# Kernel optimization log

Measured on AMD Instinct MI355X. Metric: run time of the kernel, lower is better.

Reference implementation:

```python
import jax, jax.numpy as jnp
import numpy as np

H = W = 256
N_VERTS = 6890
N_FACES = 13776
CHUNK = 164            # 13776 = 84 * 164
N_CHUNKS = N_FACES // CHUNK
BIG = 1e9
EPS = 1e-8


def _project(cam, verts):
    # weak-perspective: s * (xy + t); flip y into image (raster) space
    xy = cam[:, None, 0:1] * (verts[:, :, :2] + cam[:, None, 1:3])
    return jnp.concatenate([xy[..., 0:1], -xy[..., 1:2], verts[:, :, 2:3]], axis=-1)  # [B,N,3]


def _rasterize(proj, faces):
    """Z-buffered rasterization. proj [B,N,3], faces [F,3] ->
    fim [B,P] int32 (face index, -1 = background), wim [B,P,3] barycentric weights."""
    B = proj.shape[0]
    P = H * W
    tri = proj[:, faces]                                   # [B,F,3,3]
    tri_c = tri.reshape(B, N_CHUNKS, CHUNK, 3, 3).transpose(1, 0, 2, 3, 4)  # [nc,B,C,3,3]
    bases = (jnp.arange(N_CHUNKS) * CHUNK).astype(jnp.int32)
    c = (jnp.arange(H, dtype=jnp.float32) + 0.5) / H * 2.0 - 1.0   # pixel centers in [-1,1]
    py, px = jnp.meshgrid(c, c, indexing='ij')
    px = px.reshape(-1)[None, :, None]                     # [1,P,1]
    py = py.reshape(-1)[None, :, None]

    def step(carry, xs):
        zbuf, fid, wim = carry
        t, base = xs                                       # t [B,CHUNK,3,3]
        v = t[:, None]                                     # [B,1,CHUNK,3,3]
        x0, y0, z0 = v[..., 0, 0], v[..., 0, 1], v[..., 0, 2]
        x1, y1, z1 = v[..., 1, 0], v[..., 1, 1], v[..., 1, 2]
        x2, y2, z2 = v[..., 2, 0], v[..., 2, 1], v[..., 2, 2]
        denom = (y1 - y2) * (x0 - x2) + (x2 - x1) * (y0 - y2)
        inv = 1.0 / jnp.where(jnp.abs(denom) < EPS, 1.0, denom)
        w0 = ((y1 - y2) * (px - x2) + (x2 - x1) * (py - y2)) * inv   # [B,P,CHUNK]
        w1 = ((y2 - y0) * (px - x2) + (x0 - x2) * (py - y2)) * inv
        w2 = 1.0 - w0 - w1
        inside = (w0 >= 0) & (w1 >= 0) & (w2 >= 0) & (jnp.abs(denom) >= EPS)
        depth = jnp.where(inside, w0 * z0 + w1 * z1 + w2 * z2, BIG)
        loc = jnp.argmin(depth, axis=-1)                   # [B,P]
        li = loc[..., None]
        dmin = jnp.take_along_axis(depth, li, -1)[..., 0]
        b0 = jnp.take_along_axis(w0, li, -1)[..., 0]
        b1 = jnp.take_along_axis(w1, li, -1)[..., 0]
        b2 = jnp.take_along_axis(w2, li, -1)[..., 0]
        bsel = jnp.stack([b0, b1, b2], axis=-1)            # [B,P,3]
        upd = dmin < zbuf
        zbuf = jnp.where(upd, dmin, zbuf)
        fid = jnp.where(upd, base + loc.astype(jnp.int32), fid)
        wim = jnp.where(upd[..., None], bsel, wim)
        return (zbuf, fid, wim), None

    init = (jnp.full((B, P), BIG, jnp.float32),
            jnp.full((B, P), -1, jnp.int32),
            jnp.zeros((B, P, 3), jnp.float32))
    (zbuf, fid, wim), _ = jax.lax.scan(step, init, (tri_c, bases))
    return fid, wim


def _grid_sample_border(img, grid):
    # torch.nn.functional.grid_sample(bilinear, padding_mode='border', align_corners=False)
    B, C, Hh, Ww = img.shape
    ix = jnp.clip(((grid[..., 0] + 1.0) * Ww - 1.0) * 0.5, 0.0, Ww - 1.0)
    iy = jnp.clip(((grid[..., 1] + 1.0) * Hh - 1.0) * 0.5, 0.0, Hh - 1.0)
    x0 = jnp.floor(ix); y0 = jnp.floor(iy)
    wx = ix - x0; wy = iy - y0
    x0i = x0.astype(jnp.int32); y0i = y0.astype(jnp.int32)
    x1i = jnp.clip(x0i + 1, 0, Ww - 1); y1i = jnp.clip(y0i + 1, 0, Hh - 1)
    b = jnp.arange(B)[:, None, None]
    Ia = img[b, :, y0i, x0i]   # [B,H,W,C]
    Ib = img[b, :, y0i, x1i]
    Ic = img[b, :, y1i, x0i]
    Id = img[b, :, y1i, x1i]
    out = (Ia * ((1 - wx) * (1 - wy))[..., None] + Ib * (wx * (1 - wy))[..., None]
           + Ic * ((1 - wx) * wy)[..., None] + Id * (wx * wy)[..., None])
    return out.transpose(0, 3, 1, 2)


def setup_inputs() -> dict:
    key = jax.random.key(0)
    k1, k2, k3, k4, k5, k6 = jax.random.split(key, 6)
    B = 2
    return {
        'src_img': jax.random.normal(k1, (B, 3, H, W), jnp.float32),
        'src_cam': jax.random.uniform(k2, (B, 3), jnp.float32),
        'src_vertices': jax.random.normal(k3, (B, N_VERTS, 3), jnp.float32),
        'tgt_cam': jax.random.uniform(k4, (B, 3), jnp.float32),
        'tgt_vertices': jax.random.normal(k5, (B, N_VERTS, 3), jnp.float32),
        'faces': jax.random.randint(k6, (N_FACES, 3), 0, N_VERTS, jnp.int32),
    }


def reference(src_img, src_cam, src_vertices, tgt_cam, tgt_vertices, faces):
    B = src_img.shape[0]
    # source faces -> projected 2D verts; flip y back (matches src_f2verts[...,1] *= -1)
    src_proj = _project(src_cam, src_vertices)
    src_f2v = src_proj[:, faces][..., 0:2]                 # [B,F,3,2]
    src_f2v = src_f2v.at[..., 1].multiply(-1.0)
    # rasterize target mesh -> face-index map + barycentric weight map
    tgt_proj = _project(tgt_cam, tgt_vertices)
    fim, wim = _rasterize(tgt_proj, faces)                 # [B,P], [B,P,3]
    fid_clip = jnp.clip(fim, 0, N_FACES - 1)
    gathered = src_f2v[jnp.arange(B)[:, None], fid_clip]   # [B,P,3,2]
    flow = jnp.sum(wim[..., None] * gathered, axis=2)      # [B,P,2]
    flow = jnp.where((fim >= 0)[..., None], flow, -2.0)    # background off-grid
    flow = flow.reshape(B, H, W, 2)
    return _grid_sample_border(src_img, flow)
```

## Files before the change

### kernel.cpp

```cpp
#include <hip/hip_runtime.h>

#pragma clang fp contract(off)

#define HH 256
#define WW 256
#define NVERTS 6890
#define NFACES 13776
#define RASTN (NFACES + 1)
#define PAD1 14336
#define LISTSTRIDE 13824
#define RCHUNK 32
#define MAXCH 432
#define SLABS 4
#define WSUB 896
#define NITER 14
#define SLABSZ (4 * WSUB)
#define NBLK 2048
#define NWAVES (NBLK * 4)
#define BIGF 1000000000.0f
#define EPSF 1e-8f

__device__ __forceinline__ float pixc(int i) {
    return __fsub_rn(__fmul_rn(__fdiv_rn(__fadd_rn((float)i, 0.5f), 256.0f), 2.0f), 1.0f);
}

__device__ __forceinline__ unsigned int fsort(float f) {
    unsigned int u = __float_as_uint(f);
    return (u & 0x80000000u) ? ~u : (u | 0x80000000u);
}


__global__ __launch_bounds__(256) void precompute_kernel(
    const float* __restrict__ src_cam, const float* __restrict__ src_verts,
    const float* __restrict__ tgt_cam, const float* __restrict__ tgt_verts,
    const int* __restrict__ faces,
    float4* __restrict__ rast64, uchar4* __restrict__ pass1,
    float4* __restrict__ eplane,
    float4* __restrict__ flowg,
    unsigned long long* __restrict__ zbuf,
    int* __restrict__ counts, int* __restrict__ done, int* __restrict__ qcount,
    int B)
{
    int idx = blockIdx.x * blockDim.x + threadIdx.x;
    if (idx < B * HH * WW) zbuf[idx] = ~0ull;
    if (counts && idx < B * 256) { counts[idx] = 0; done[idx] = 0; }
    if (qcount && idx == 0) qcount[0] = 0;
    if (idx >= B * PAD1) return;
    int b = idx / PAD1;
    int f = idx - b * PAD1;
    if (f >= NFACES) {
        if (pass1) pass1[(size_t)b * PAD1 + f] = make_uchar4(255, 255, 0, 0);
        if (f == NFACES) {
            float4* rr = rast64 + ((size_t)b * RASTN + f) * 4;
            rr[0] = make_float4(0.0f, 0.0f, 0.0f, 0.0f);
            rr[1] = make_float4(0.0f, 0.0f, 1.0f, __int_as_float(-1));
            rr[2] = make_float4(BIGF, BIGF, BIGF, 0.0f);
            rr[3] = make_float4(0.0f, 0.0f, 0.0f, 0.0f);
        }
        return;
    }
    float4* rr = rast64 + ((size_t)b * RASTN + f) * 4;
    int i0 = faces[3*f+0], i1 = faces[3*f+1], i2 = faces[3*f+2];

    float tc0 = tgt_cam[3*b+0], tc1 = tgt_cam[3*b+1], tc2 = tgt_cam[3*b+2];
    const float* tv = tgt_verts + (size_t)b * NVERTS * 3;
    float x0 = __fmul_rn(tc0, __fadd_rn(tv[3*i0+0], tc1));
    float y0 = -__fmul_rn(tc0, __fadd_rn(tv[3*i0+1], tc2));
    float z0 = tv[3*i0+2];
    float x1 = __fmul_rn(tc0, __fadd_rn(tv[3*i1+0], tc1));
    float y1 = -__fmul_rn(tc0, __fadd_rn(tv[3*i1+1], tc2));
    float z1 = tv[3*i1+2];
    float x2 = __fmul_rn(tc0, __fadd_rn(tv[3*i2+0], tc1));
    float y2 = -__fmul_rn(tc0, __fadd_rn(tv[3*i2+1], tc2));
    float z2 = tv[3*i2+2];

    float A  = __fsub_rn(y1, y2);
    float D  = __fsub_rn(x0, x2);
    float Bc = __fsub_rn(x2, x1);
    float E_ = __fsub_rn(y0, y2);
    float denom = __fadd_rn(__fmul_rn(A, D), __fmul_rn(Bc, E_));
    bool valid = (fabsf(denom) >= EPSF);
    float inv = __fdiv_rn(1.0f, valid ? denom : 1.0f);
    float Cc = __fsub_rn(y2, y0);

    if (valid) {
        rr[0] = make_float4(x2, y2, A, Bc);
        rr[1] = make_float4(Cc, D, inv, __int_as_float(f));
        rr[2] = make_float4(z0, z1, z2, 0.0f);
    } else {
        rr[0] = make_float4(0.0f, 0.0f, 0.0f, 0.0f);
        rr[1] = make_float4(0.0f, 0.0f, 1.0f, __int_as_float(f));
        rr[2] = make_float4(BIGF, BIGF, BIGF, 0.0f);
    }
    rr[3] = make_float4(0.0f, 0.0f, 0.0f, 0.0f);

    uchar4 range;
    float4 e1, e2, e3;
    if (valid) {
        float xmn = fminf(fminf(x0, x1), x2), xmx = fmaxf(fmaxf(x0, x1), x2);
        float ymn = fminf(fminf(y0, y1), y2), ymx = fmaxf(fmaxf(y0, y1), y2);
        float S = fmaxf(fmaxf(fabsf(xmn), fabsf(xmx)),
                        fmaxf(fabsf(ymn), fabsf(ymx))) + 1.01f;
        float slop = 2e-6f * S;
        float l0 = sqrtf(D*D + E_*E_);
        float dx1v = x1 - x2, dy1v = y1 - y2;
        float l1 = sqrtf(dx1v*dx1v + dy1v*dy1v);
        float dx2v = x1 - x0, dy2v = y1 - y0;
        float l2 = sqrtf(dx2v*dx2v + dy2v*dy2v);
        float mp = fmaxf(fmaxf(l0*l1, l1*l2), l0*l2);
        float Ex = slop * mp / fabsf(denom);
        float m = Ex + slop + 1e-4f;
        float bxmn = xmn - m, bymn = ymn - m, bxmx = xmx + m, bymx = ymx + m;

        int txlo = (int)floorf((__fmul_rn(__fadd_rn(bxmn, 1.0f), 128.0f) - 15.5f) * 0.0625f);
        txlo = max(0, min(16, txlo));
        while (txlo > 0  && pixc(16*(txlo-1)+15) >= bxmn) txlo--;
        while (txlo < 16 && pixc(16*txlo+15)     <  bxmn) txlo++;
        int txhi = (int)floorf((__fmul_rn(__fadd_rn(bxmx, 1.0f), 128.0f) - 0.5f) * 0.0625f);
        txhi = max(-1, min(15, txhi));
        while (txhi < 15 && pixc(16*(txhi+1)) <= bxmx) txhi++;
        while (txhi >= 0 && pixc(16*txhi)     >  bxmx) txhi--;
        int tylo = (int)floorf((__fmul_rn(__fadd_rn(bymn, 1.0f), 128.0f) - 15.5f) * 0.0625f);
        tylo = max(0, min(16, tylo));
        while (tylo > 0  && pixc(16*(tylo-1)+15) >= bymn) tylo--;
        while (tylo < 16 && pixc(16*tylo+15)     <  bymn) tylo++;
        int tyhi = (int)floorf((__fmul_rn(__fadd_rn(bymx, 1.0f), 128.0f) - 0.5f) * 0.0625f);
        tyhi = max(-1, min(15, tyhi));
        while (tyhi < 15 && pixc(16*(tyhi+1)) <= bymx) tyhi++;
        while (tyhi >= 0 && pixc(16*tyhi)     >  bymx) tyhi--;
        if (txlo > txhi || tylo > tyhi || txlo > 15 || tylo > 15 ||
            txhi < 0 || tyhi < 0) {
            range = make_uchar4(255, 255, 0, 0);
        } else {
            range = make_uchar4((unsigned char)txlo, (unsigned char)tylo,
                                (unsigned char)txhi, (unsigned char)tyhi);
        }

        float s = (denom >= 0.0f) ? 1.0f : -1.0f;
        float gx0 = s * A,  gy0 = s * Bc;
        float gx1 = s * Cc, gy1 = s * D;
        float gx2 = s * (y0 - y1), gy2 = s * (x1 - x0);
        float b0 = -(gx0 * x2 + gy0 * y2);
        float b1 = -(gx1 * x2 + gy1 * y2);
        float b2 = fabsf(denom) - b0 - b1;
        float mm15 = 1.5f * m;
        float k0 = b0 + mm15 * l1 + 1e-6f;
        float k1 = b1 + mm15 * l0 + 1e-6f;
        float k2 = b2 + mm15 * l2 + 1e-6f;
        e1 = make_float4(gx0, gy0, k0, gx1);
        e2 = make_float4(gy1, k1, gx2, gy2);
        e3 = make_float4(k2, 0.0f, 0.0f, 0.0f);
    } else {
        range = make_uchar4(255, 255, 0, 0);
        e1 = make_float4(0.0f, 0.0f, -1.0f, 0.0f);
        e2 = make_float4(0.0f, -1.0f, 0.0f, 0.0f);
        e3 = make_float4(-1.0f, 0.0f, 0.0f, 0.0f);
    }
    if (pass1) pass1[(size_t)b * PAD1 + f] = range;
    if (eplane) {
        float4* ep = eplane + ((size_t)b * NFACES + f) * 4;
        ep[0] = e1; ep[1] = e2; ep[2] = e3;
        ep[3] = make_float4(0.0f, 0.0f, 0.0f, 0.0f);
    }

    float sc0 = src_cam[3*b+0], sc1 = src_cam[3*b+1], sc2 = src_cam[3*b+2];
    const float* sv = src_verts + (size_t)b * NVERTS * 3;
    float g0x = __fmul_rn(sc0, __fadd_rn(sv[3*i0+0], sc1));
    float g0y = __fmul_rn(sc0, __fadd_rn(sv[3*i0+1], sc2));
    float g1x = __fmul_rn(sc0, __fadd_rn(sv[3*i1+0], sc1));
    float g1y = __fmul_rn(sc0, __fadd_rn(sv[3*i1+1], sc2));
    float g2x = __fmul_rn(sc0, __fadd_rn(sv[3*i2+0], sc1));
    float g2y = __fmul_rn(sc0, __fadd_rn(sv[3*i2+1], sc2));
    size_t fo = ((size_t)b * NFACES + f) * 2;
    flowg[fo+0] = make_float4(g0x, g0y, g1x, g1y);
    flowg[fo+1] = make_float4(g2x, g2y, 0.0f, 0.0f);
}

__global__ __launch_bounds__(256) void bin_kernel(
    const uchar4* __restrict__ pass1, const float4* __restrict__ eplane,
    int* __restrict__ lists,
    int* __restrict__ counts, int* __restrict__ done,
    unsigned int* __restrict__ queue, int* __restrict__ qcount, int B)
{
    __shared__ int seg[4][WSUB];
    int tile = blockIdx.x;
    int slab = blockIdx.y;
    int b = blockIdx.z;
    int tileG = b * 256 + tile;
    int tX = tile & 15, tY = tile >> 4;
    float txmin = pixc(tX * 16), txmax = pixc(tX * 16 + 15);
    float tymin = pixc(tY * 16), tymax = pixc(tY * 16 + 15);

    int wv = threadIdx.x >> 6, lane = threadIdx.x & 63;
    const uchar4* p1 = pass1 + (size_t)b * PAD1;
    const float4* ep = eplane + (size_t)b * NFACES * 4;
    int* mylist = lists + (size_t)tileG * LISTSTRIDE;
    int wlo = slab * SLABSZ + wv * WSUB;
    int cnt = 0;

    int f0 = wlo + lane;
    uchar4 c = p1[f0];

    #pragma unroll
    for (int it = 0; it < NITER; ++it) {
        uchar4 n;
        if (it + 1 < NITER) n = p1[f0 + (it + 1) * 64];
        int f = f0 + it * 64;
        bool pass = (tX >= (int)c.x) & (tX <= (int)c.z) &
                    (tY >= (int)c.y) & (tY <= (int)c.w);
        unsigned long long m = __ballot(pass);
        if (pass) {
            int pre = __popcll(m & ((1ull << lane) - 1ull));
            seg[wv][cnt + pre] = f;
        }
        cnt += __popcll(m);
        c = n;
    }

    int outc = 0;
    for (int base = 0; base < cnt; base += 64) {
        int i = base + lane;
        int f = (i < cnt) ? seg[wv][i] : 0;
        const float4* er = ep + (size_t)f * 4;
        float4 e1 = er[0], e2 = er[1], e3 = er[2];
        float v0 = e1.x * (e1.x >= 0.0f ? txmax : txmin)
                 + e1.y * (e1.y >= 0.0f ? tymax : tymin) + e1.z;
        float v1 = e1.w * (e1.w >= 0.0f ? txmax : txmin)
                 + e2.x * (e2.x >= 0.0f ? tymax : tymin) + e2.y;
        float v2 = e2.z * (e2.z >= 0.0f ? txmax : txmin)
                 + e2.w * (e2.w >= 0.0f ? tymax : tymin) + e3.x;
        bool pass = (i < cnt) & (v0 >= 0.0f) & (v1 >= 0.0f) & (v2 >= 0.0f);
        unsigned long long m = __ballot(pass);
        if (pass) {
            int pre = __popcll(m & ((1ull << lane) - 1ull));
            seg[wv][outc + pre] = f;
        }
        outc += __popcll(m);
    }
    cnt = outc;

    int gbase = 0;
    if (lane == 0 && cnt) gbase = atomicAdd(&counts[tileG], cnt);
    gbase = __shfl(gbase, 0);
    for (int i = lane; i < cnt; i += 64) mylist[gbase + i] = seg[wv][i];

    __syncthreads();
    if (threadIdx.x < 64) {
        int isLast = 0, cc = 0;
        if (threadIdx.x == 0) {
            isLast = (atomicAdd(&done[tileG], 1) == SLABS - 1);
            if (isLast) cc = atomicAdd(&counts[tileG], 0);
        }
        isLast = __shfl(isLast, 0);
        if (isLast) {
            cc = __shfl(cc, 0);
            int padded = (cc + RCHUNK - 1) & ~(RCHUNK - 1);
            for (int i = cc + threadIdx.x; i < padded; i += 64)
                mylist[i] = NFACES;
            int nch = padded / RCHUNK;
            if (nch) {
                int qb = 0;
                if (threadIdx.x == 0) qb = atomicAdd(qcount, nch);
                qb = __shfl(qb, 0);
                for (int kk = threadIdx.x; kk < nch; kk += 64)
                    queue[qb + kk] = ((unsigned int)tileG << 10) | (unsigned int)kk;
            }
        }
    }
}

__global__ __launch_bounds__(256) void raster_kernel(
    const float* __restrict__ rast64, const int* __restrict__ lists,
    const unsigned int* __restrict__ queue, const int* __restrict__ qcount,
    unsigned long long* __restrict__ zbuf, int B)
{
    int wv = threadIdx.x >> 6, lane = threadIdx.x & 63;
    int waveId = blockIdx.x * 4 + wv;
    int qn = queue ? qcount[0] : B * 256 * MAXCH;
    qn = __builtin_amdgcn_readfirstlane(qn);

    for (int e = waveId; e < qn; e += NWAVES) {
        int tileG, k;
        if (queue) {
            unsigned int ent = queue[e];
            tileG = (int)(ent >> 10); k = (int)(ent & 1023u);
        } else {
            tileG = e / MAXCH; k = e - tileG * MAXCH;
        }
        tileG = __builtin_amdgcn_readfirstlane(tileG);
        k = __builtin_amdgcn_readfirstlane(k);
        int b = tileG >> 8, tile = tileG & 255;
        const int* lp = lists ? (lists + (size_t)tileG * LISTSTRIDE + k * RCHUNK)
                              : nullptr;
        const float* rb = rast64 + (size_t)b * RASTN * 16;

        int tX = tile & 15, tY = tile >> 4;
        int col = lane & 15, row0 = lane >> 4;
        int pxi = tX * 16 + col;
        float px = pixc(pxi);
        float py0 = pixc(tY * 16 + row0);
        float py1 = pixc(tY * 16 + row0 + 4);
        float py2 = pixc(tY * 16 + row0 + 8);
        float py3 = pixc(tY * 16 + row0 + 12);

        float z0c = BIGF, z1c = BIGF, z2c = BIGF, z3c = BIGF;
        int f0c = -1, f1c = -1, f2c = -1, f3c = -1;

        for (int j = 0; j < RCHUNK; j += 4) {
            int4 fis;
            if (lp) {
                fis = *(const int4*)(lp + j);
            } else {
                int base = k * RCHUNK + j;
                fis.x = min(base + 0, NFACES); fis.y = min(base + 1, NFACES);
                fis.z = min(base + 2, NFACES); fis.w = min(base + 3, NFACES);
            }
            #pragma unroll
            for (int q = 0; q < 4; ++q) {
                int fi = (q == 0) ? fis.x : (q == 1) ? fis.y : (q == 2) ? fis.z : fis.w;
                fi = __builtin_amdgcn_readfirstlane(fi);
                const float* r = rb + (size_t)fi * 16;
                float X2 = r[0], Y2 = r[1], A = r[2], Bc = r[3];
                float Cc = r[4], Dd = r[5], inv = r[6];
                int   fid = __float_as_int(r[7]);
                float Z0 = r[8], Z1 = r[9], Z2 = r[10];

                float dx  = __fsub_rn(px, X2);
                float Adx = __fmul_rn(A, dx);
                float Cdx = __fmul_rn(Cc, dx);
                auto evalp = [&](float py, float& zc, int& fc) {
                    float dy = __fsub_rn(py, Y2);
                    float w0 = __fmul_rn(__fadd_rn(Adx, __fmul_rn(Bc, dy)), inv);
                    float w1 = __fmul_rn(__fadd_rn(Cdx, __fmul_rn(Dd, dy)), inv);
                    float w2 = __fsub_rn(__fsub_rn(1.0f, w0), w1);
                    float d  = __fadd_rn(__fadd_rn(__fmul_rn(w0, Z0), __fmul_rn(w1, Z1)),
                                         __fmul_rn(w2, Z2));
                    float mm = fminf(fminf(w0, w1), w2);
                    bool ins = (mm >= 0.0f) & (d < zc);
                    if (ins) { zc = d; fc = fid; }
                };
                evalp(py0, z0c, f0c);
                evalp(py1, z1c, f1c);
                evalp(py2, z2c, f2c);
                evalp(py3, z3c, f3c);
            }
        }

        auto commit = [&](int rowk, float zc, int fc) {
            if (fc >= 0) {
                unsigned long long pk =
                    ((unsigned long long)fsort(zc) << 32) | (unsigned int)fc;
                int pyi = tY * 16 + row0 + rowk * 4;
                atomicMin(&zbuf[((size_t)b << 16) | (pyi << 8) | pxi], pk);
            }
        };
        commit(0, z0c, f0c);
        commit(1, z1c, f1c);
        commit(2, z2c, f2c);
        commit(3, z3c, f3c);
    }
}

__global__ __launch_bounds__(256) void resolve_kernel(
    const float* __restrict__ rast64, const float4* __restrict__ flowg,
    const unsigned long long* __restrict__ zbuf,
    const float* __restrict__ src_img, float* __restrict__ out, int B)
{
    int idx = blockIdx.x * 256 + threadIdx.x;
    if (idx >= B * HH * WW) return;
    int b = idx >> 16;
    int pix = idx & 65535;
    int pxi = pix & 255, pyi = pix >> 8;
    float px = pixc(pxi), py = pixc(pyi);

    unsigned int fid = (unsigned int)zbuf[idx];
    float fx, fy;
    if (fid != 0xFFFFFFFFu) {
        const float* r = rast64 + ((size_t)b * RASTN + fid) * 16;
        float dx = __fsub_rn(px, r[0]);
        float dy = __fsub_rn(py, r[1]);
        float w0 = __fmul_rn(__fadd_rn(__fmul_rn(r[2], dx), __fmul_rn(r[3], dy)), r[6]);
        float w1 = __fmul_rn(__fadd_rn(__fmul_rn(r[4], dx), __fmul_rn(r[5], dy)), r[6]);
        float w2 = __fsub_rn(__fsub_rn(1.0f, w0), w1);
        const float4* fg = flowg + ((size_t)b * NFACES + fid) * 2;
        float4 g0 = fg[0];
        float4 g1 = fg[1];
        fx = __fadd_rn(__fadd_rn(__fmul_rn(w0, g0.x), __fmul_rn(w1, g0.z)),
                       __fmul_rn(w2, g1.x));
        fy = __fadd_rn(__fadd_rn(__fmul_rn(w0, g0.y), __fmul_rn(w1, g0.w)),
                       __fmul_rn(w2, g1.y));
    } else {
        fx = -2.0f; fy = -2.0f;
    }

    float ix = __fmul_rn(__fsub_rn(__fmul_rn(__fadd_rn(fx, 1.0f), 256.0f), 1.0f), 0.5f);
    float iy = __fmul_rn(__fsub_rn(__fmul_rn(__fadd_rn(fy, 1.0f), 256.0f), 1.0f), 0.5f);
    ix = fminf(fmaxf(ix, 0.0f), 255.0f);
    iy = fminf(fmaxf(iy, 0.0f), 255.0f);
    float x0f = floorf(ix), y0f = floorf(iy);
    float wx = __fsub_rn(ix, x0f), wy = __fsub_rn(iy, y0f);
    int x0i = (int)x0f, y0i = (int)y0f;
    int x1i = min(x0i + 1, 255), y1i = min(y0i + 1, 255);
    float omwx = __fsub_rn(1.0f, wx), omwy = __fsub_rn(1.0f, wy);
    float wa = __fmul_rn(omwx, omwy);
    float wb = __fmul_rn(wx, omwy);
    float wc = __fmul_rn(omwx, wy);
    float wd = __fmul_rn(wx, wy);
    const float* img = src_img + (size_t)b * 3 * HH * WW;
    int o00 = y0i * WW + x0i, o01 = y0i * WW + x1i;
    int o10 = y1i * WW + x0i, o11 = y1i * WW + x1i;
    float* ob = out + (size_t)b * 3 * HH * WW + (size_t)pyi * WW + pxi;
    for (int c = 0; c < 3; ++c) {
        const float* ic = img + (size_t)c * HH * WW;
        float Ia = ic[o00], Ib = ic[o01], Ic = ic[o10], Id = ic[o11];
        float val = __fadd_rn(__fadd_rn(__fadd_rn(__fmul_rn(Ia, wa), __fmul_rn(Ib, wb)),
                                        __fmul_rn(Ic, wc)),
                              __fmul_rn(Id, wd));
        ob[(size_t)c * HH * WW] = val;
    }
}

extern "C" void kernel_launch(void* const* d_in, const int* in_sizes, int n_in,
                              void* d_out, int out_size, void* d_ws, size_t ws_size,
                              hipStream_t stream)
{
    const float* src_img   = (const float*)d_in[0];
    const float* src_cam   = (const float*)d_in[1];
    const float* src_verts = (const float*)d_in[2];
    const float* tgt_cam   = (const float*)d_in[3];
    const float* tgt_verts = (const float*)d_in[4];
    const int*   faces     = (const int*)d_in[5];
    int B = in_sizes[1] / 3;

    size_t off = 0;
    auto alloc = [&](size_t bytes) {
        size_t o = off;
        off = (off + bytes + 255) & ~(size_t)255;
        return o;
    };
    size_t rastOff = alloc((size_t)B * RASTN * 64);
    size_t p1Off   = alloc((size_t)B * PAD1 * 4);
    size_t edgOff  = alloc((size_t)B * NFACES * 64);
    size_t flowOff = alloc((size_t)B * NFACES * 2 * sizeof(float4));
    size_t zbufOff = alloc((size_t)B * HH * WW * sizeof(unsigned long long));
    size_t cntOff  = alloc((size_t)B * 256 * sizeof(int));
    size_t donOff  = alloc((size_t)B * 256 * sizeof(int));
    size_t qcOff   = alloc(sizeof(int));
    size_t quOff   = alloc((size_t)B * 256 * MAXCH * sizeof(unsigned int));
    size_t listOff = alloc((size_t)B * 256 * LISTSTRIDE * sizeof(int));
    bool binned = (off <= ws_size);

    char* ws = (char*)d_ws;
    float4* rast64 = (float4*)(ws + rastOff);
    uchar4* pass1  = binned ? (uchar4*)(ws + p1Off)  : nullptr;
    float4* eplane = binned ? (float4*)(ws + edgOff) : nullptr;
    float4* flowg  = (float4*)(ws + flowOff);
    unsigned long long* zbuf = (unsigned long long*)(ws + zbufOff);
    int* counts = binned ? (int*)(ws + cntOff) : nullptr;
    int* done   = binned ? (int*)(ws + donOff) : nullptr;
    int* qcount = binned ? (int*)(ws + qcOff)  : nullptr;
    unsigned int* queue = binned ? (unsigned int*)(ws + quOff) : nullptr;
    int* lists  = binned ? (int*)(ws + listOff) : nullptr;

    int nInit = B * HH * WW;
    int nPre  = B * PAD1;
    int nMax  = nInit > nPre ? nInit : nPre;
    precompute_kernel<<<(nMax + 255) / 256, 256, 0, stream>>>(
        src_cam, src_verts, tgt_cam, tgt_verts, faces,
        rast64, pass1, eplane, flowg, zbuf, counts, done, qcount, B);
    if (binned) {
        bin_kernel<<<dim3(256, SLABS, B), 256, 0, stream>>>(
            pass1, eplane, lists, counts, done, queue, qcount, B);
    }
    raster_kernel<<<NBLK, 256, 0, stream>>>(
        (const float*)rast64, lists, queue, qcount, zbuf, B);
    resolve_kernel<<<(B * HH * WW + 255) / 256, 256, 0, stream>>>(
        (const float*)rast64, flowg, zbuf, src_img, (float*)d_out, B);
}
```

Baseline: 147.1 us.

## Add per-face min-depth culling against zbuf and reorder raster work chunk-major

Each face stores a conservative minimum depth, and the raster waves read the current zbuf values for their pixels up front. They skip a face's barycentric evaluation when no lane's depth bound could be beaten, updating that bound after each chunk. The atomic work queue is replaced by a chunk-major enumeration using a max chunk count plus the per-tile padded count, so all tiles' first chunks run first and populate zbuf early. This adds atomic loads and empty iterations for tiles with fewer chunks, and culling depends on a safe epsilon margin.

```diff
diff --git a/kernel.cpp b/kernel.cpp
--- a/kernel.cpp
+++ b/kernel.cpp
@@ -27,6 +27,12 @@
 __device__ __forceinline__ unsigned int fsort(float f) {
     unsigned int u = __float_as_uint(f);
     return (u & 0x80000000u) ? ~u : (u | 0x80000000u);
+}
+
+__device__ __forceinline__ float funsort(unsigned int u) {
+    if (u == 0xFFFFFFFFu) return BIGF;
+    unsigned int v = (u & 0x80000000u) ? (u & 0x7FFFFFFFu) : ~u;
+    return __uint_as_float(v);
 }
 
 
@@ -55,7 +61,7 @@
             rr[0] = make_float4(0.0f, 0.0f, 0.0f, 0.0f);
             rr[1] = make_float4(0.0f, 0.0f, 1.0f, __int_as_float(-1));
             rr[2] = make_float4(BIGF, BIGF, BIGF, 0.0f);
-            rr[3] = make_float4(0.0f, 0.0f, 0.0f, 0.0f);
+            rr[3] = make_float4(BIGF, 0.0f, 0.0f, 0.0f);
         }
         return;
     }
@@ -83,16 +89,20 @@
     float inv = __fdiv_rn(1.0f, valid ? denom : 1.0f);
     float Cc = __fsub_rn(y2, y0);
 
+    float fzmin = fminf(fminf(z0, z1), z2)
+                - 4e-6f * (fabsf(z0) + fabsf(z1) + fabsf(z2)) - 1e-30f;
+
     if (valid) {
         rr[0] = make_float4(x2, y2, A, Bc);
         rr[1] = make_float4(Cc, D, inv, __int_as_float(f));
         rr[2] = make_float4(z0, z1, z2, 0.0f);
+        rr[3] = make_float4(fzmin, 0.0f, 0.0f, 0.0f);
     } else {
         rr[0] = make_float4(0.0f, 0.0f, 0.0f, 0.0f);
         rr[1] = make_float4(0.0f, 0.0f, 1.0f, __int_as_float(f));
         rr[2] = make_float4(BIGF, BIGF, BIGF, 0.0f);
-    }
-    rr[3] = make_float4(0.0f, 0.0f, 0.0f, 0.0f);
+        rr[3] = make_float4(BIGF, 0.0f, 0.0f, 0.0f);
+    }
 
     uchar4 range;
     float4 e1, e2, e3;
@@ -180,7 +190,7 @@
     const uchar4* __restrict__ pass1, const float4* __restrict__ eplane,
     int* __restrict__ lists,
     int* __restrict__ counts, int* __restrict__ done,
-    unsigned int* __restrict__ queue, int* __restrict__ qcount, int B)
+    int* __restrict__ qcount, int B)
 {
     __shared__ int seg[4][WSUB];
     int tile = blockIdx.x;
@@ -257,13 +267,10 @@
             int padded = (cc + RCHUNK - 1) & ~(RCHUNK - 1);
             for (int i = cc + threadIdx.x; i < padded; i += 64)
                 mylist[i] = NFACES;
-            int nch = padded / RCHUNK;
-            if (nch) {
-                int qb = 0;
-                if (threadIdx.x == 0) qb = atomicAdd(qcount, nch);
-                qb = __shfl(qb, 0);
-                for (int kk = threadIdx.x; kk < nch; kk += 64)
-                    queue[qb + kk] = ((unsigned int)tileG << 10) | (unsigned int)kk;
+            if (threadIdx.x == 0) {
+                int nch = padded / RCHUNK;
+                if (nch) atomicMax(qcount, nch);
+                done[tileG] = padded;
             }
         }
     }
@@ -271,37 +278,54 @@
 
 __global__ __launch_bounds__(256) void raster_kernel(
     const float* __restrict__ rast64, const int* __restrict__ lists,
-    const unsigned int* __restrict__ queue, const int* __restrict__ qcount,
+    const int* __restrict__ donep, const int* __restrict__ qcount,
     unsigned long long* __restrict__ zbuf, int B)
 {
     int wv = threadIdx.x >> 6, lane = threadIdx.x & 63;
     int waveId = blockIdx.x * 4 + wv;
-    int qn = queue ? qcount[0] : B * 256 * MAXCH;
-    qn = __builtin_amdgcn_readfirstlane(qn);
+    int NT = B * 256;
+    int maxK = lists ? qcount[0] : MAXCH;
+    maxK = __builtin_amdgcn_readfirstlane(maxK);
+    int qn = maxK * NT;
 
     for (int e = waveId; e < qn; e += NWAVES) {
-        int tileG, k;
-        if (queue) {
-            unsigned int ent = queue[e];
-            tileG = (int)(ent >> 10); k = (int)(ent & 1023u);
-        } else {
-            tileG = e / MAXCH; k = e - tileG * MAXCH;
-        }
+        int k = e / NT;
+        int tileG = e - k * NT;
+        k = __builtin_amdgcn_readfirstlane(k);
         tileG = __builtin_amdgcn_readfirstlane(tileG);
-        k = __builtin_amdgcn_readfirstlane(k);
+        const int* lp = nullptr;
+        if (lists) {
+            int padded = donep[tileG];
+            if (k * RCHUNK >= padded) continue;
+            lp = lists + (size_t)tileG * LISTSTRIDE + k * RCHUNK;
+        }
         int b = tileG >> 8, tile = tileG & 255;
-        const int* lp = lists ? (lists + (size_t)tileG * LISTSTRIDE + k * RCHUNK)
-                              : nullptr;
         const float* rb = rast64 + (size_t)b * RASTN * 16;
 
         int tX = tile & 15, tY = tile >> 4;
         int col = lane & 15, row0 = lane >> 4;
         int pxi = tX * 16 + col;
         float px = pixc(pxi);
-        float py0 = pixc(tY * 16 + row0);
-        float py1 = pixc(tY * 16 + row0 + 4);
-        float py2 = pixc(tY * 16 + row0 + 8);
-        float py3 = pixc(tY * 16 + row0 + 12);
+        int ry0 = tY * 16 + row0;
+        float py0 = pixc(ry0);
+        float py1 = pixc(ry0 + 4);
+        float py2 = pixc(ry0 + 8);
+        float py3 = pixc(ry0 + 12);
+
+        size_t zbase = ((size_t)b << 16) | (size_t)pxi;
+        unsigned long long pk0 = __hip_atomic_load(
+            &zbuf[zbase | ((size_t)ry0 << 8)], __ATOMIC_RELAXED, __HIP_MEMORY_SCOPE_AGENT);
+        unsigned long long pk1 = __hip_atomic_load(
+            &zbuf[zbase | ((size_t)(ry0 + 4) << 8)], __ATOMIC_RELAXED, __HIP_MEMORY_SCOPE_AGENT);
+        unsigned long long pk2 = __hip_atomic_load(
+            &zbuf[zbase | ((size_t)(ry0 + 8) << 8)], __ATOMIC_RELAXED, __HIP_MEMORY_SCOPE_AGENT);
+        unsigned long long pk3 = __hip_atomic_load(
+            &zbuf[zbase | ((size_t)(ry0 + 12) << 8)], __ATOMIC_RELAXED, __HIP_MEMORY_SCOPE_AGENT);
+        float zb0 = funsort((unsigned int)(pk0 >> 32));
+        float zb1 = funsort((unsigned int)(pk1 >> 32));
+        float zb2 = funsort((unsigned int)(pk2 >> 32));
+        float zb3 = funsort((unsigned int)(pk3 >> 32));
+        float laneBound = fmaxf(fmaxf(zb0, zb1), fmaxf(zb2, zb3));
 
         float z0c = BIGF, z1c = BIGF, z2c = BIGF, z3c = BIGF;
         int f0c = -1, f1c = -1, f2c = -1, f3c = -1;
@@ -320,37 +344,42 @@
                 int fi = (q == 0) ? fis.x : (q == 1) ? fis.y : (q == 2) ? fis.z : fis.w;
                 fi = __builtin_amdgcn_readfirstlane(fi);
                 const float* r = rb + (size_t)fi * 16;
-                float X2 = r[0], Y2 = r[1], A = r[2], Bc = r[3];
-                float Cc = r[4], Dd = r[5], inv = r[6];
-                int   fid = __float_as_int(r[7]);
-                float Z0 = r[8], Z1 = r[9], Z2 = r[10];
-
-                float dx  = __fsub_rn(px, X2);
-                float Adx = __fmul_rn(A, dx);
-                float Cdx = __fmul_rn(Cc, dx);
-                auto evalp = [&](float py, float& zc, int& fc) {
-                    float dy = __fsub_rn(py, Y2);
-                    float w0 = __fmul_rn(__fadd_rn(Adx, __fmul_rn(Bc, dy)), inv);
-                    float w1 = __fmul_rn(__fadd_rn(Cdx, __fmul_rn(Dd, dy)), inv);
-                    float w2 = __fsub_rn(__fsub_rn(1.0f, w0), w1);
-                    float d  = __fadd_rn(__fadd_rn(__fmul_rn(w0, Z0), __fmul_rn(w1, Z1)),
-                                         __fmul_rn(w2, Z2));
-                    float mm = fminf(fminf(w0, w1), w2);
-                    bool ins = (mm >= 0.0f) & (d < zc);
-                    if (ins) { zc = d; fc = fid; }
-                };
-                evalp(py0, z0c, f0c);
-                evalp(py1, z1c, f1c);
-                evalp(py2, z2c, f2c);
-                evalp(py3, z3c, f3c);
+                float fzmin = r[12];
+                if (__any(fzmin <= laneBound)) {
+                    float X2 = r[0], Y2 = r[1], A = r[2], Bc = r[3];
+                    float Cc = r[4], Dd = r[5], inv = r[6];
+                    int   fid = __float_as_int(r[7]);
+                    float Z0 = r[8], Z1 = r[9], Z2 = r[10];
+
+                    float dx  = __fsub_rn(px, X2);
+                    float Adx = __fmul_rn(A, dx);
+                    float Cdx = __fmul_rn(Cc, dx);
+                    auto evalp = [&](float py, float& zc, int& fc) {
+                        float dy = __fsub_rn(py, Y2);
+                        float w0 = __fmul_rn(__fadd_rn(Adx, __fmul_rn(Bc, dy)), inv);
+                        float w1 = __fmul_rn(__fadd_rn(Cdx, __fmul_rn(Dd, dy)), inv);
+                        float w2 = __fsub_rn(__fsub_rn(1.0f, w0), w1);
+                        float d  = __fadd_rn(__fadd_rn(__fmul_rn(w0, Z0), __fmul_rn(w1, Z1)),
+                                             __fmul_rn(w2, Z2));
+                        float mm = fminf(fminf(w0, w1), w2);
+                        bool ins = (mm >= 0.0f) & (d < zc);
+                        if (ins) { zc = d; fc = fid; }
+                    };
+                    evalp(py0, z0c, f0c);
+                    evalp(py1, z1c, f1c);
+                    evalp(py2, z2c, f2c);
+                    evalp(py3, z3c, f3c);
+                }
             }
+            laneBound = fmaxf(fmaxf(fminf(zb0, z0c), fminf(zb1, z1c)),
+                              fmaxf(fminf(zb2, z2c), fminf(zb3, z3c)));
         }
 
         auto commit = [&](int rowk, float zc, int fc) {
             if (fc >= 0) {
                 unsigned long long pk =
                     ((unsigned long long)fsort(zc) << 32) | (unsigned int)fc;
-                int pyi = tY * 16 + row0 + rowk * 4;
+                int pyi = ry0 + rowk * 4;
                 atomicMin(&zbuf[((size_t)b << 16) | (pyi << 8) | pxi], pk);
             }
         };
@@ -446,7 +475,6 @@
     size_t cntOff  = alloc((size_t)B * 256 * sizeof(int));
     size_t donOff  = alloc((size_t)B * 256 * sizeof(int));
     size_t qcOff   = alloc(sizeof(int));
-    size_t quOff   = alloc((size_t)B * 256 * MAXCH * sizeof(unsigned int));
     size_t listOff = alloc((size_t)B * 256 * LISTSTRIDE * sizeof(int));
     bool binned = (off <= ws_size);
 
@@ -459,7 +487,6 @@
     int* counts = binned ? (int*)(ws + cntOff) : nullptr;
     int* done   = binned ? (int*)(ws + donOff) : nullptr;
     int* qcount = binned ? (int*)(ws + qcOff)  : nullptr;
-    unsigned int* queue = binned ? (unsigned int*)(ws + quOff) : nullptr;
     int* lists  = binned ? (int*)(ws + listOff) : nullptr;
 
     int nInit = B * HH * WW;
@@ -470,10 +497,10 @@
         rast64, pass1, eplane, flowg, zbuf, counts, done, qcount, B);
     if (binned) {
         bin_kernel<<<dim3(256, SLABS, B), 256, 0, stream>>>(
-            pass1, eplane, lists, counts, done, queue, qcount, B);
+            pass1, eplane, lists, counts, done, qcount, B);
     }
     raster_kernel<<<NBLK, 256, 0, stream>>>(
-        (const float*)rast64, lists, queue, qcount, zbuf, B);
+        (const float*)rast64, lists, done, qcount, zbuf, B);
     resolve_kernel<<<(B * HH * WW + 255) / 256, 256, 0, stream>>>(
         (const float*)rast64, flowg, zbuf, src_img, (float*)d_out, B);
 }
```

Result: slower. 285.4 us (+94.0%).

## Add seed raster pass and per-chunk depth culling against zbuf

Applied to the files above, without the earlier changes.

Adds a per-face conservative minimum depth array and a seeding raster launch that rasterizes the first chunk of every tile first. The main raster pass then reads the current zbuf depths for its 64 pixels, takes the tile-wave maximum, and skips faces whose minimum depth cannot beat it, skipping whole chunks when none survive. This is meant to cut barycentric evaluation work in overdrawn tiles, at the cost of an extra kernel launch, extra zbuf reads per chunk and a serialized seed phase.

```diff
diff --git a/kernel.cpp b/kernel.cpp
--- a/kernel.cpp
+++ b/kernel.cpp
@@ -16,7 +16,7 @@
 #define NITER 14
 #define SLABSZ (4 * WSUB)
 #define NBLK 2048
-#define NWAVES (NBLK * 4)
+#define NBLKSEED 128
 #define BIGF 1000000000.0f
 #define EPSF 1e-8f
 
@@ -27,6 +27,12 @@
 __device__ __forceinline__ unsigned int fsort(float f) {
     unsigned int u = __float_as_uint(f);
     return (u & 0x80000000u) ? ~u : (u | 0x80000000u);
+}
+
+__device__ __forceinline__ float funsort(unsigned int u) {
+    if (u == 0xFFFFFFFFu) return BIGF;
+    unsigned int v = (u & 0x80000000u) ? (u & 0x7FFFFFFFu) : ~u;
+    return __uint_as_float(v);
 }
 
 
@@ -34,7 +40,8 @@
     const float* __restrict__ src_cam, const float* __restrict__ src_verts,
     const float* __restrict__ tgt_cam, const float* __restrict__ tgt_verts,
     const int* __restrict__ faces,
-    float4* __restrict__ rast64, uchar4* __restrict__ pass1,
+    float4* __restrict__ rast64, float* __restrict__ fz,
+    uchar4* __restrict__ pass1,
     float4* __restrict__ eplane,
     float4* __restrict__ flowg,
     unsigned long long* __restrict__ zbuf,
@@ -56,6 +63,7 @@
             rr[1] = make_float4(0.0f, 0.0f, 1.0f, __int_as_float(-1));
             rr[2] = make_float4(BIGF, BIGF, BIGF, 0.0f);
             rr[3] = make_float4(0.0f, 0.0f, 0.0f, 0.0f);
+            if (fz) fz[(size_t)b * RASTN + f] = BIGF;
         }
         return;
     }
@@ -83,6 +91,9 @@
     float inv = __fdiv_rn(1.0f, valid ? denom : 1.0f);
     float Cc = __fsub_rn(y2, y0);
 
+    float fzmin = fminf(fminf(z0, z1), z2)
+                - 4e-6f * (fabsf(z0) + fabsf(z1) + fabsf(z2)) - 1e-30f;
+
     if (valid) {
         rr[0] = make_float4(x2, y2, A, Bc);
         rr[1] = make_float4(Cc, D, inv, __int_as_float(f));
@@ -93,6 +104,7 @@
         rr[2] = make_float4(BIGF, BIGF, BIGF, 0.0f);
     }
     rr[3] = make_float4(0.0f, 0.0f, 0.0f, 0.0f);
+    if (fz) fz[(size_t)b * RASTN + f] = valid ? fzmin : BIGF;
 
     uchar4 range;
     float4 e1, e2, e3;
@@ -258,55 +270,100 @@
             for (int i = cc + threadIdx.x; i < padded; i += 64)
                 mylist[i] = NFACES;
             int nch = padded / RCHUNK;
-            if (nch) {
+            if (nch > 1) {
                 int qb = 0;
-                if (threadIdx.x == 0) qb = atomicAdd(qcount, nch);
+                if (threadIdx.x == 0) qb = atomicAdd(qcount, nch - 1);
                 qb = __shfl(qb, 0);
-                for (int kk = threadIdx.x; kk < nch; kk += 64)
-                    queue[qb + kk] = ((unsigned int)tileG << 10) | (unsigned int)kk;
+                for (int kk = 1 + threadIdx.x; kk < nch; kk += 64)
+                    queue[qb + kk - 1] =
+                        ((unsigned int)tileG << 10) | (unsigned int)kk;
             }
+            if (threadIdx.x == 0)
+                done[tileG] = padded;
         }
     }
 }
 
 __global__ __launch_bounds__(256) void raster_kernel(
     const float* __restrict__ rast64, const int* __restrict__ lists,
-    const unsigned int* __restrict__ queue, const int* __restrict__ qcount,
-    unsigned long long* __restrict__ zbuf, int B)
+    const float* __restrict__ fz,
+    const unsigned int* __restrict__ queue, const int* __restrict__ donep,
+    const int* __restrict__ qcount,
+    unsigned long long* __restrict__ zbuf, int B, int seedMode)
 {
     int wv = threadIdx.x >> 6, lane = threadIdx.x & 63;
     int waveId = blockIdx.x * 4 + wv;
-    int qn = queue ? qcount[0] : B * 256 * MAXCH;
+    int nwaves = gridDim.x * 4;
+    int NT = B * 256;
+    int qn;
+    if (!lists)        qn = B * 256 * MAXCH;
+    else if (seedMode) qn = NT;
+    else               qn = qcount[0];
     qn = __builtin_amdgcn_readfirstlane(qn);
 
-    for (int e = waveId; e < qn; e += NWAVES) {
+    for (int e = waveId; e < qn; e += nwaves) {
         int tileG, k;
-        if (queue) {
+        if (!lists) {
+            tileG = e / MAXCH; k = e - tileG * MAXCH;
+        } else if (seedMode) {
+            tileG = e; k = 0;
+            if (donep[tileG] == 0) continue;
+        } else {
             unsigned int ent = queue[e];
             tileG = (int)(ent >> 10); k = (int)(ent & 1023u);
-        } else {
-            tileG = e / MAXCH; k = e - tileG * MAXCH;
         }
         tileG = __builtin_amdgcn_readfirstlane(tileG);
         k = __builtin_amdgcn_readfirstlane(k);
-        int b = tileG >> 8, tile = tileG & 255;
         const int* lp = lists ? (lists + (size_t)tileG * LISTSTRIDE + k * RCHUNK)
                               : nullptr;
+        int b = tileG >> 8, tile = tileG & 255;
         const float* rb = rast64 + (size_t)b * RASTN * 16;
 
         int tX = tile & 15, tY = tile >> 4;
         int col = lane & 15, row0 = lane >> 4;
         int pxi = tX * 16 + col;
         float px = pixc(pxi);
-        float py0 = pixc(tY * 16 + row0);
-        float py1 = pixc(tY * 16 + row0 + 4);
-        float py2 = pixc(tY * 16 + row0 + 8);
-        float py3 = pixc(tY * 16 + row0 + 12);
+        int ry0 = tY * 16 + row0;
+        float py0 = pixc(ry0);
+        float py1 = pixc(ry0 + 4);
+        float py2 = pixc(ry0 + 8);
+        float py3 = pixc(ry0 + 12);
+
+        unsigned int mask = 0xFFFFFFFFu;
+        if (lists && !seedMode) {
+            size_t zbase = ((size_t)b << 16) | (size_t)pxi;
+            unsigned long long pk0 = __hip_atomic_load(
+                &zbuf[zbase | ((size_t)ry0 << 8)],
+                __ATOMIC_RELAXED, __HIP_MEMORY_SCOPE_AGENT);
+            unsigned long long pk1 = __hip_atomic_load(
+                &zbuf[zbase | ((size_t)(ry0 + 4) << 8)],
+                __ATOMIC_RELAXED, __HIP_MEMORY_SCOPE_AGENT);
+            unsigned long long pk2 = __hip_atomic_load(
+                &zbuf[zbase | ((size_t)(ry0 + 8) << 8)],
+                __ATOMIC_RELAXED, __HIP_MEMORY_SCOPE_AGENT);
+            unsigned long long pk3 = __hip_atomic_load(
+                &zbuf[zbase | ((size_t)(ry0 + 12) << 8)],
+                __ATOMIC_RELAXED, __HIP_MEMORY_SCOPE_AGENT);
+            float lb = fmaxf(fmaxf(funsort((unsigned int)(pk0 >> 32)),
+                                   funsort((unsigned int)(pk1 >> 32))),
+                             fmaxf(funsort((unsigned int)(pk2 >> 32)),
+                                   funsort((unsigned int)(pk3 >> 32))));
+            #pragma unroll
+            for (int off = 1; off < 64; off <<= 1)
+                lb = fmaxf(lb, __shfl_xor(lb, off, 64));
+            int fidx = lp[lane & 31];
+            float fzv = fz[(size_t)b * RASTN + fidx];
+            unsigned long long bm = __ballot((lane < 32) & (fzv <= lb));
+            mask = (unsigned int)bm;
+            if (mask == 0u) continue;
+        }
 
         float z0c = BIGF, z1c = BIGF, z2c = BIGF, z3c = BIGF;
         int f0c = -1, f1c = -1, f2c = -1, f3c = -1;
 
         for (int j = 0; j < RCHUNK; j += 4) {
+            unsigned int g = (mask >> j) & 0xFu;
+            if (!g) continue;
             int4 fis;
             if (lp) {
                 fis = *(const int4*)(lp + j);
@@ -317,6 +374,7 @@
             }
             #pragma unroll
             for (int q = 0; q < 4; ++q) {
+                if (!(g & (1u << q))) continue;
                 int fi = (q == 0) ? fis.x : (q == 1) ? fis.y : (q == 2) ? fis.z : fis.w;
                 fi = __builtin_amdgcn_readfirstlane(fi);
                 const float* r = rb + (size_t)fi * 16;
@@ -350,7 +408,7 @@
             if (fc >= 0) {
                 unsigned long long pk =
                     ((unsigned long long)fsort(zc) << 32) | (unsigned int)fc;
-                int pyi = tY * 16 + row0 + rowk * 4;
+                int pyi = ry0 + rowk * 4;
                 atomicMin(&zbuf[((size_t)b << 16) | (pyi << 8) | pxi], pk);
             }
         };
@@ -439,6 +497,7 @@
         return o;
     };
     size_t rastOff = alloc((size_t)B * RASTN * 64);
+    size_t fzOff   = alloc((size_t)B * RASTN * sizeof(float));
     size_t p1Off   = alloc((size_t)B * PAD1 * 4);
     size_t edgOff  = alloc((size_t)B * NFACES * 64);
     size_t flowOff = alloc((size_t)B * NFACES * 2 * sizeof(float4));
@@ -452,6 +511,7 @@
 
     char* ws = (char*)d_ws;
     float4* rast64 = (float4*)(ws + rastOff);
+    float*  fz     = (float*)(ws + fzOff);
     uchar4* pass1  = binned ? (uchar4*)(ws + p1Off)  : nullptr;
     float4* eplane = binned ? (float4*)(ws + edgOff) : nullptr;
     float4* flowg  = (float4*)(ws + flowOff);
@@ -467,13 +527,19 @@
     int nMax  = nInit > nPre ? nInit : nPre;
     precompute_kernel<<<(nMax + 255) / 256, 256, 0, stream>>>(
         src_cam, src_verts, tgt_cam, tgt_verts, faces,
-        rast64, pass1, eplane, flowg, zbuf, counts, done, qcount, B);
+        rast64, fz, pass1, eplane, flowg, zbuf, counts, done, qcount, B);
     if (binned) {
         bin_kernel<<<dim3(256, SLABS, B), 256, 0, stream>>>(
             pass1, eplane, lists, counts, done, queue, qcount, B);
-    }
-    raster_kernel<<<NBLK, 256, 0, stream>>>(
-        (const float*)rast64, lists, queue, qcount, zbuf, B);
+        raster_kernel<<<NBLKSEED, 256, 0, stream>>>(
+            (const float*)rast64, lists, fz, queue, done, qcount, zbuf, B, 1);
+        raster_kernel<<<NBLK, 256, 0, stream>>>(
+            (const float*)rast64, lists, fz, queue, done, qcount, zbuf, B, 0);
+    } else {
+        raster_kernel<<<NBLK, 256, 0, stream>>>(
+            (const float*)rast64, nullptr, fz, nullptr, nullptr, nullptr,
+            zbuf, B, 0);
+    }
     resolve_kernel<<<(B * HH * WW + 255) / 256, 256, 0, stream>>>(
         (const float*)rast64, flowg, zbuf, src_img, (float*)d_out, B);
 }
```

Result: slower. 154.3 us (+4.9%).
